# Kernel tuning notes

Measured on AMD Instinct MI355X. Metric: run time of the kernel, lower is better.

Reference implementation:

```python
import jax, jax.numpy as jnp
import numpy as np

SQRT_DIM = np.sqrt(64.0).astype(np.float32)
NEG_INF = -1000000000.0


def setup_inputs() -> dict:
    key = jax.random.key(0)
    kq, kk, kv = jax.random.split(key, 3)
    B, H, S, D = 4, 8, 2048, 64
    q = jax.random.normal(kq, (B, H, S, D), dtype=jnp.float32)
    k = jax.random.normal(kk, (B, H, S, D), dtype=jnp.float32)
    v = jax.random.normal(kv, (B, H, S, D), dtype=jnp.float32)
    mask = jnp.ones((B, 1, S, S), dtype=jnp.int32)
    return {"q": q, "k": k, "v": v, "mask": mask}


def reference(q, k, v, mask):
    # scores: [B, H, S, S]
    attn = jnp.einsum("bhqd,bhkd->bhqk", q, k) / SQRT_DIM
    attn = jnp.where(mask == 0, NEG_INF, attn)
    attn = jax.nn.softmax(attn, axis=-1)
    # dropout p=0.0 -> identity
    output = jnp.einsum("bhqk,bhkd->bhqd", attn, v)
    return (output, attn)
```

## Files before the change

### kernel.cpp

```cpp
#include <hip/hip_runtime.h>
#include <hip/hip_bf16.h>
#include <stdint.h>

#define NB 4
#define NH 8
#define SDIM 2048
#define DDIM 64

#define KSCALE 0.18033688011112042f

typedef short s8v __attribute__((ext_vector_type(8)));
typedef float f4v __attribute__((ext_vector_type(4)));

__device__ __forceinline__ float bf2f(unsigned short h) {
    union { unsigned int u; float f; } c; c.u = ((unsigned int)h) << 16; return c.f;
}
__device__ __forceinline__ unsigned short f2bf(float x) {
    union { float f; unsigned int u; } c; c.f = x;
    return (unsigned short)((c.u + 0x7FFFu + ((c.u >> 16) & 1u)) >> 16);
}

__global__ void sdpa_prep_cast_k(const float* __restrict__ k, unsigned short* __restrict__ kb) {
    int i = blockIdx.x * 256 + threadIdx.x;
    float4 v = ((const float4*)k)[i];
    ushort4 o;
    o.x = f2bf(v.x * KSCALE);
    o.y = f2bf(v.y * KSCALE);
    o.z = f2bf(v.z * KSCALE);
    o.w = f2bf(v.w * KSCALE);
    ((ushort4*)kb)[i] = o;
}

__global__ void sdpa_prep_transpose_v(const float* __restrict__ v, unsigned short* __restrict__ vt) {
    __shared__ float t[64][65];
    const int bh = blockIdx.x >> 5;
    const int kt = blockIdx.x & 31;
    const int tid = threadIdx.x;
    const float* src = v + ((size_t)bh * SDIM + (size_t)kt * 64) * DDIM;
    #pragma unroll
    for (int i = 0; i < 4; ++i) {
        int idx = i * 256 + tid;
        int kl = idx >> 4, c4 = idx & 15;
        float4 val = ((const float4*)(src + kl * DDIM))[c4];
        t[kl][c4 * 4 + 0] = val.x; t[kl][c4 * 4 + 1] = val.y;
        t[kl][c4 * 4 + 2] = val.z; t[kl][c4 * 4 + 3] = val.w;
    }
    __syncthreads();
    const int d   = tid >> 2;
    const int klb = (tid & 3) << 4;
    unsigned short* dst = vt + ((size_t)bh * DDIM + d) * SDIM + kt * 64 + klb;
    #pragma unroll
    for (int c = 0; c < 4; ++c) {
        ushort4 w;
        w.x = f2bf(t[klb + c * 4 + 0][d]);
        w.y = f2bf(t[klb + c * 4 + 1][d]);
        w.z = f2bf(t[klb + c * 4 + 2][d]);
        w.w = f2bf(t[klb + c * 4 + 3][d]);
        ((ushort4*)dst)[c] = w;
    }
}

__launch_bounds__(512, 4)
__global__ void sdpa_main(const float* __restrict__ q,
                          const unsigned short* __restrict__ kb,
                          const unsigned short* __restrict__ vtb,
                          const int* __restrict__ mask,
                          float* __restrict__ outO,
                          float* __restrict__ outP) {
    extern __shared__ char lds[];
    unsigned short* sc = (unsigned short*)lds;

    const int bx = blockIdx.x;
    const int bh = bx >> 7;
    const int q0 = (bx & 127) << 4;
    const int b  = bh >> 3;

    const int tid  = threadIdx.x;
    const int wave = tid >> 6;
    const int lane = tid & 63;
    const int l15  = lane & 15;
    const int quad = lane >> 4;

    s8v aq0, aq1;
    {
        const float* qr = q + ((size_t)bh * SDIM + q0 + l15) * DDIM + quad * 8;
        float4 x0 = ((const float4*)qr)[0];
        float4 x1 = ((const float4*)qr)[1];
        float4 y0 = ((const float4*)(qr + 32))[0];
        float4 y1 = ((const float4*)(qr + 32))[1];
        aq0[0]=(short)f2bf(x0.x); aq0[1]=(short)f2bf(x0.y); aq0[2]=(short)f2bf(x0.z); aq0[3]=(short)f2bf(x0.w);
        aq0[4]=(short)f2bf(x1.x); aq0[5]=(short)f2bf(x1.y); aq0[6]=(short)f2bf(x1.z); aq0[7]=(short)f2bf(x1.w);
        aq1[0]=(short)f2bf(y0.x); aq1[1]=(short)f2bf(y0.y); aq1[2]=(short)f2bf(y0.z); aq1[3]=(short)f2bf(y0.w);
        aq1[4]=(short)f2bf(y1.x); aq1[5]=(short)f2bf(y1.y); aq1[6]=(short)f2bf(y1.z); aq1[7]=(short)f2bf(y1.w);
    }

    {
        const unsigned short* kbase = kb + (size_t)bh * SDIM * DDIM;
        const int n_start = wave << 8;
        #pragma unroll 2
        for (int t = 0; t < 16; ++t) {
            const int n0 = n_start + (t << 4);
            const unsigned short* krow = kbase + (size_t)(n0 + l15) * DDIM + quad * 8;
            s8v b0 = *(const s8v*)(krow);
            s8v b1 = *(const s8v*)(krow + 32);
            f4v acc = {0.f, 0.f, 0.f, 0.f};
            acc = __builtin_amdgcn_mfma_f32_16x16x32_bf16(aq0, b0, acc, 0, 0, 0);
            acc = __builtin_amdgcn_mfma_f32_16x16x32_bf16(aq1, b1, acc, 0, 0, 0);
            const int col = n0 + l15;
            const int blk = col >> 3;
            const int off = col & 7;
            #pragma unroll
            for (int r = 0; r < 4; ++r) {
                int row = quad * 4 + r;
                sc[row * 2048 + (((blk ^ row) << 3) | off)] = f2bf(acc[r]);
            }
        }
    }

    const int* mbase = mask + (size_t)b * SDIM * SDIM + (size_t)q0 * SDIM;
    int4 ma[8];
    {
        const int4* mrow = (const int4*)(mbase + (size_t)wave * SDIM);
        #pragma unroll
        for (int i = 0; i < 4; ++i) {
            const int blk = lane + (i << 6);
            ma[2 * i + 0] = mrow[blk * 2 + 0];
            ma[2 * i + 1] = mrow[blk * 2 + 1];
        }
    }
    __syncthreads();

    #pragma unroll
    for (int pass = 0; pass < 2; ++pass) {
        const int row = wave + (pass << 3);
        unsigned short* scrow = sc + row * 2048;

        float s[32];
        float rmax = -3.0e38f;
        #pragma unroll
        for (int i = 0; i < 4; ++i) {
            const int blk = lane + (i << 6);
            s8v vv = *(const s8v*)(scrow + ((blk ^ row) << 3));
            const int4 m0 = ma[2 * i + 0];
            const int4 m1 = ma[2 * i + 1];
            const int mm[8] = { m0.x, m0.y, m0.z, m0.w, m1.x, m1.y, m1.z, m1.w };
            #pragma unroll
            for (int e = 0; e < 8; ++e) {
                float x = bf2f((unsigned short)vv[e]);
                x = (mm[e] == 0) ? -1.0e9f : x;
                s[i * 8 + e] = x;
                rmax = fmaxf(rmax, x);
            }
        }
        if (pass == 0) {
            const int4* mrow = (const int4*)(mbase + (size_t)(wave + 8) * SDIM);
            #pragma unroll
            for (int i = 0; i < 4; ++i) {
                const int blk = lane + (i << 6);
                ma[2 * i + 0] = mrow[blk * 2 + 0];
                ma[2 * i + 1] = mrow[blk * 2 + 1];
            }
        }
        #pragma unroll
        for (int d = 1; d < 64; d <<= 1) rmax = fmaxf(rmax, __shfl_xor(rmax, d));

        float rsum = 0.f;
        #pragma unroll
        for (int i = 0; i < 32; ++i) {
            float e = exp2f(s[i] - rmax);
            s[i] = e;
            rsum += e;
        }
        #pragma unroll
        for (int d = 1; d < 64; d <<= 1) rsum += __shfl_xor(rsum, d);
        const float rinv = 1.0f / rsum;

        float* prow = outP + (size_t)bh * SDIM * SDIM + (size_t)(q0 + row) * SDIM;
        #pragma unroll
        for (int i = 0; i < 4; ++i) {
            const int blk = lane + (i << 6);
            float p0 = s[i*8+0] * rinv, p1 = s[i*8+1] * rinv;
            float p2 = s[i*8+2] * rinv, p3 = s[i*8+3] * rinv;
            float p4 = s[i*8+4] * rinv, p5 = s[i*8+5] * rinv;
            float p6 = s[i*8+6] * rinv, p7 = s[i*8+7] * rinv;
            f4v o0 = { p0, p1, p2, p3 };
            f4v o1 = { p4, p5, p6, p7 };
            __builtin_nontemporal_store(o0, (f4v*)prow + blk * 2 + 0);
            __builtin_nontemporal_store(o1, (f4v*)prow + blk * 2 + 1);
            s8v vv;
            vv[0]=(short)f2bf(p0); vv[1]=(short)f2bf(p1); vv[2]=(short)f2bf(p2); vv[3]=(short)f2bf(p3);
            vv[4]=(short)f2bf(p4); vv[5]=(short)f2bf(p5); vv[6]=(short)f2bf(p6); vv[7]=(short)f2bf(p7);
            *(s8v*)(scrow + ((blk ^ row) << 3)) = vv;
        }
    }
    __syncthreads();

    {
        const int dt = wave & 3;
        const int kh = wave >> 2;
        const unsigned short* vbase = vtb + ((size_t)bh * DDIM + (dt << 4) + l15) * SDIM
                                          + (kh << 10) + quad * 8;
        const unsigned short* arow = sc + l15 * 2048;
        f4v acc0 = {0,0,0,0}, acc1 = {0,0,0,0};
        #pragma unroll 4
        for (int ks = 0; ks < 32; ++ks) {
            const int k0 = (kh << 10) + (ks << 5);
            s8v a  = *(const s8v*)(arow + ((((k0 >> 3) + quad) ^ l15) << 3));
            s8v bb = *(const s8v*)(vbase + (ks << 5));
            if (ks & 1) acc1 = __builtin_amdgcn_mfma_f32_16x16x32_bf16(a, bb, acc1, 0, 0, 0);
            else        acc0 = __builtin_amdgcn_mfma_f32_16x16x32_bf16(a, bb, acc0, 0, 0, 0);
        }
        f4v acc = acc0 + acc1;

        __syncthreads();
        float* scratch = (float*)lds;
        if (kh == 1) {
            #pragma unroll
            for (int r = 0; r < 4; ++r)
                scratch[(dt << 8) + ((quad * 4 + r) << 4) + l15] = acc[r];
        }
        __syncthreads();
        if (kh == 0) {
            float* orow = outO + ((size_t)bh * SDIM + q0) * DDIM + (dt << 4) + l15;
            #pragma unroll
            for (int r = 0; r < 4; ++r)
                orow[(quad * 4 + r) * DDIM] = acc[r] + scratch[(dt << 8) + ((quad * 4 + r) << 4) + l15];
        }
    }
}

extern "C" void kernel_launch(void* const* d_in, const int* in_sizes, int n_in,
                              void* d_out, int out_size, void* d_ws, size_t ws_size,
                              hipStream_t stream) {
    const float* q  = (const float*)d_in[0];
    const float* k  = (const float*)d_in[1];
    const float* v  = (const float*)d_in[2];
    const int* mask = (const int*)d_in[3];

    const size_t qkv_elems = (size_t)NB * NH * SDIM * DDIM;
    float* outO = (float*)d_out;
    float* outP = (float*)d_out + qkv_elems;

    unsigned short* kb  = (unsigned short*)d_ws;
    unsigned short* vtb = kb + qkv_elems;

    sdpa_prep_cast_k<<<(int)(qkv_elems / 1024), 256, 0, stream>>>(k, kb);
    sdpa_prep_transpose_v<<<NB * NH * (SDIM / 64), 256, 0, stream>>>(v, vtb);
    sdpa_main<<<NB * NH * (SDIM / 16), 512, 65536, stream>>>(q, kb, vtb, mask, outO, outP);
}
```

Before: 842.8 us.

## Pack int32 mask into bitmask in prep kernel and read bits in main

Adds a prep kernel that compresses the int32 mask [B,1,S,S] into one bit per element. The main kernel then reads 32-bit words instead of int4 vectors. Before, every head's blocks re-read the full 4-byte-per-element mask, so mask traffic was repeated across all 8 heads; now the mask is read once and the main kernel's mask reads become tiny. It also swaps the manual float-to-bf16 rounding for the __bf16 conversion intrinsic. The cost is an extra launch and one full pass over the mask.

```diff
diff --git a/kernel.cpp b/kernel.cpp
--- a/kernel.cpp
+++ b/kernel.cpp
@@ -16,8 +16,7 @@
     union { unsigned int u; float f; } c; c.u = ((unsigned int)h) << 16; return c.f;
 }
 __device__ __forceinline__ unsigned short f2bf(float x) {
-    union { float f; unsigned int u; } c; c.f = x;
-    return (unsigned short)((c.u + 0x7FFFu + ((c.u >> 16) & 1u)) >> 16);
+    union { __bf16 b; unsigned short u; } c; c.b = (__bf16)x; return c.u;
 }
 
 __global__ void sdpa_prep_cast_k(const float* __restrict__ k, unsigned short* __restrict__ kb) {
@@ -60,11 +59,26 @@
     }
 }
 
+__global__ void sdpa_prep_pack_mask(const int* __restrict__ mask, unsigned* __restrict__ bm) {
+    int t = blockIdx.x * 256 + threadIdx.x;
+    const int4* src = (const int4*)mask + (size_t)t * 8;
+    unsigned w = 0;
+    #pragma unroll
+    for (int i = 0; i < 8; ++i) {
+        int4 m = src[i];
+        w |= (m.x != 0 ? 1u : 0u) << (4 * i + 0);
+        w |= (m.y != 0 ? 1u : 0u) << (4 * i + 1);
+        w |= (m.z != 0 ? 1u : 0u) << (4 * i + 2);
+        w |= (m.w != 0 ? 1u : 0u) << (4 * i + 3);
+    }
+    bm[t] = w;
+}
+
 __launch_bounds__(512, 4)
 __global__ void sdpa_main(const float* __restrict__ q,
                           const unsigned short* __restrict__ kb,
                           const unsigned short* __restrict__ vtb,
-                          const int* __restrict__ mask,
+                          const unsigned* __restrict__ bm,
                           float* __restrict__ outO,
                           float* __restrict__ outP) {
     extern __shared__ char lds[];
@@ -116,49 +130,34 @@
             }
         }
     }
-
-    const int* mbase = mask + (size_t)b * SDIM * SDIM + (size_t)q0 * SDIM;
-    int4 ma[8];
-    {
-        const int4* mrow = (const int4*)(mbase + (size_t)wave * SDIM);
-        #pragma unroll
-        for (int i = 0; i < 4; ++i) {
-            const int blk = lane + (i << 6);
-            ma[2 * i + 0] = mrow[blk * 2 + 0];
-            ma[2 * i + 1] = mrow[blk * 2 + 1];
-        }
-    }
     __syncthreads();
+
+    const unsigned* bmbase = bm + ((size_t)b * SDIM + q0) * 64;
+    const int sh = (lane & 3) << 3;
 
     #pragma unroll
     for (int pass = 0; pass < 2; ++pass) {
         const int row = wave + (pass << 3);
         unsigned short* scrow = sc + row * 2048;
 
+        const unsigned* brow = bmbase + row * 64;
+        unsigned wm[4];
+        #pragma unroll
+        for (int i = 0; i < 4; ++i) wm[i] = brow[(lane >> 2) + (i << 4)] >> sh;
+
         float s[32];
         float rmax = -3.0e38f;
         #pragma unroll
         for (int i = 0; i < 4; ++i) {
             const int blk = lane + (i << 6);
             s8v vv = *(const s8v*)(scrow + ((blk ^ row) << 3));
-            const int4 m0 = ma[2 * i + 0];
-            const int4 m1 = ma[2 * i + 1];
-            const int mm[8] = { m0.x, m0.y, m0.z, m0.w, m1.x, m1.y, m1.z, m1.w };
+            const unsigned w = wm[i];
             #pragma unroll
             for (int e = 0; e < 8; ++e) {
                 float x = bf2f((unsigned short)vv[e]);
-                x = (mm[e] == 0) ? -1.0e9f : x;
+                x = ((w >> e) & 1u) ? x : -1.0e9f;
                 s[i * 8 + e] = x;
                 rmax = fmaxf(rmax, x);
-            }
-        }
-        if (pass == 0) {
-            const int4* mrow = (const int4*)(mbase + (size_t)(wave + 8) * SDIM);
-            #pragma unroll
-            for (int i = 0; i < 4; ++i) {
-                const int blk = lane + (i << 6);
-                ma[2 * i + 0] = mrow[blk * 2 + 0];
-                ma[2 * i + 1] = mrow[blk * 2 + 1];
             }
         }
         #pragma unroll
@@ -243,8 +242,10 @@
 
     unsigned short* kb  = (unsigned short*)d_ws;
     unsigned short* vtb = kb + qkv_elems;
+    unsigned* bmw       = (unsigned*)(vtb + qkv_elems);
 
     sdpa_prep_cast_k<<<(int)(qkv_elems / 1024), 256, 0, stream>>>(k, kb);
     sdpa_prep_transpose_v<<<NB * NH * (SDIM / 64), 256, 0, stream>>>(v, vtb);
-    sdpa_main<<<NB * NH * (SDIM / 16), 512, 65536, stream>>>(q, kb, vtb, mask, outO, outP);
-}
+    sdpa_prep_pack_mask<<<NB * SDIM * 64 / 256, 256, 0, stream>>>(mask, bmw);
+    sdpa_main<<<NB * NH * (SDIM / 16), 512, 65536, stream>>>(q, kb, vtb, bmw, outO, outP);
+}
```

New measurement: 861.5 us. 1.02x slower.
